# Kernel tuning notes

Hardware: AMD Instinct MI355X
Metric: run time of the kernel (lower is better)

## Reference

```python
import jax, jax.numpy as jnp
import numpy as np

B, T, N_EMBD, HEAD = 4, 4096, 1024, 64


def setup_inputs() -> dict:
    key = jax.random.key(0)
    kx, kk, kq, kv = jax.random.split(key, 4)
    x = jax.random.normal(kx, (B, T, N_EMBD), dtype=jnp.float32)
    s = 1.0 / np.sqrt(N_EMBD)  # init scale so activations stay O(1)
    Wk = jax.random.normal(kk, (N_EMBD, HEAD), dtype=jnp.float32) * s
    Wq = jax.random.normal(kq, (N_EMBD, HEAD), dtype=jnp.float32) * s
    Wv = jax.random.normal(kv, (N_EMBD, HEAD), dtype=jnp.float32) * s
    return {"x": x, "Wk": Wk, "Wq": Wq, "Wv": Wv}


def reference(x, Wk, Wq, Wv):
    Bd, Td, C = x.shape
    k = jnp.einsum('btc,ch->bth', x, Wk)
    q = jnp.einsum('btc,ch->bth', x, Wq)
    v = jnp.einsum('btc,ch->bth', x, Wv)
    # scores scaled by C**-0.5 where C = n_embd (as in the source, not head_size)
    w = jnp.einsum('bth,bsh->bts', q, k) * (C ** -0.5)
    causal = jnp.tril(jnp.ones((Td, Td), dtype=bool))  # [T, T]
    w = jnp.where(causal, w, -jnp.inf)
    w = jax.nn.softmax(w, axis=-1)
    out = jnp.einsum('bts,bsh->bth', w, v)  # [B, T, head_size]
    return out
```

## Files before the change

kernel.cpp:

```cpp
#include <hip/hip_runtime.h>
#include <cmath>

#define NB 4
#define NT 4096
#define NC 1024
#define NH 64
#define SCALE 0.03125f
#define MFIX 3.0f
#define LOG2E 1.4426950408889634f
#define NSPLIT 8
#define QE 1048576

typedef __attribute__((ext_vector_type(8))) short v8s;
typedef __attribute__((ext_vector_type(4))) float f32x4;

static __device__ __forceinline__ ushort f2bf(float x) {
    union { float f; uint u; } c; c.f = x;
    return (ushort)((c.u + 0x7FFF + ((c.u >> 16) & 1)) >> 16);
}
static __device__ __forceinline__ float bf2f(ushort h) {
    union { uint u; float f; } c; c.u = (uint)h << 16;
    return c.f;
}
static __device__ __forceinline__ uint pk2bf(float hi_f, float lo_f) {
    uint uh = __float_as_uint(hi_f) + 0x8000u;
    uint ul = __float_as_uint(lo_f) + 0x8000u;
    return __builtin_amdgcn_perm(uh, ul, 0x07060302u);
}

__global__ __launch_bounds__(256) void prep_kernel(
    const float* __restrict__ Wk, const float* __restrict__ Wq,
    const float* __restrict__ Wv, ushort* __restrict__ Wb)
{
    const int g    = blockIdx.x * 256 + threadIdx.x;
    const int lane = g & 63;
    const int kc   = (g >> 6) & 31;
    const int nt   = g >> 11;
    const int n    = nt * 16 + (lane & 15);
    const float* W = (n < 64) ? Wq : (n < 128) ? Wk : Wv;
    const int col  = n & 63;
    const int k0   = kc * 32 + ((lane >> 4) << 3);
    ushort t8[8];
    #pragma unroll
    for (int j = 0; j < 8; ++j)
        t8[j] = f2bf(W[(k0 + j) * 64 + col]);
    *(uint4*)(Wb + (size_t)g * 8) = *(const uint4*)t8;
}

#define PPAD 72

__global__ __launch_bounds__(256) void proj_kernel(
    const float* __restrict__ x, const ushort* __restrict__ Wb,
    ushort* __restrict__ qpack, ushort* __restrict__ kpack,
    ushort* __restrict__ vpack)
{
    __shared__ __align__(16) ushort As[2][32 * PPAD];
    __shared__ __align__(16) ushort Cs[32][200];

    const int tid  = threadIdx.x;
    const int w    = tid >> 6;
    const int lane = tid & 63;
    const int ln   = lane & 15;
    const int quad = lane >> 4;
    const long r0  = (long)blockIdx.x * 32;

    const int arow = tid >> 3, acol = (tid & 7) * 8;
    const float* xs = x + (r0 + arow) * NC + acol;

    const ushort* wb0 = Wb + (size_t)(w * 3 + 0) * 16384 + lane * 8;
    const ushort* wb1 = Wb + (size_t)(w * 3 + 1) * 16384 + lane * 8;
    const ushort* wb2 = Wb + (size_t)(w * 3 + 2) * 16384 + lane * 8;

    f32x4 acc[2][3];
    #pragma unroll
    for (int s = 0; s < 2; ++s)
        #pragma unroll
        for (int nt = 0; nt < 3; ++nt) acc[s][nt] = (f32x4){0.f,0.f,0.f,0.f};

    float4 f0 = *(const float4*)(xs);
    float4 f1 = *(const float4*)(xs + 4);
    float4 g0 = *(const float4*)(xs + 64);
    float4 g1 = *(const float4*)(xs + 68);
    v8s b[3][2];
    b[0][0] = *(const v8s*)(wb0);       b[0][1] = *(const v8s*)(wb0 + 512);
    b[1][0] = *(const v8s*)(wb1);       b[1][1] = *(const v8s*)(wb1 + 512);
    b[2][0] = *(const v8s*)(wb2);       b[2][1] = *(const v8s*)(wb2 + 512);
    {
        uint4 p = { pk2bf(f0.y, f0.x), pk2bf(f0.w, f0.z),
                    pk2bf(f1.y, f1.x), pk2bf(f1.w, f1.z) };
        *(uint4*)(&As[0][arow * PPAD + acol]) = p;
    }
    __syncthreads();

    int buf = 0;
    #pragma unroll
    for (int it = 0; it < 16; ++it) {
        float4 h0, h1;
        v8s nb[3][2];
        if (it < 14) {
            const int k2 = (it + 2) * 64;
            h0 = *(const float4*)(xs + k2);
            h1 = *(const float4*)(xs + k2 + 4);
        }
        if (it < 15) {
            const int off = (it + 1) * 1024;
            nb[0][0] = *(const v8s*)(wb0 + off); nb[0][1] = *(const v8s*)(wb0 + off + 512);
            nb[1][0] = *(const v8s*)(wb1 + off); nb[1][1] = *(const v8s*)(wb1 + off + 512);
            nb[2][0] = *(const v8s*)(wb2 + off); nb[2][1] = *(const v8s*)(wb2 + off + 512);
        }

        #pragma unroll
        for (int s = 0; s < 2; ++s) {
            const ushort* ap = &As[buf][(s * 16 + ln) * PPAD + quad * 8];
            v8s a0 = *(const v8s*)(ap);
            v8s a1 = *(const v8s*)(ap + 32);
            #pragma unroll
            for (int nt = 0; nt < 3; ++nt) {
                acc[s][nt] = __builtin_amdgcn_mfma_f32_16x16x32_bf16(a0, b[nt][0], acc[s][nt], 0, 0, 0);
                acc[s][nt] = __builtin_amdgcn_mfma_f32_16x16x32_bf16(a1, b[nt][1], acc[s][nt], 0, 0, 0);
            }
        }

        if (it < 15) {
            uint4 p = { pk2bf(g0.y, g0.x), pk2bf(g0.w, g0.z),
                        pk2bf(g1.y, g1.x), pk2bf(g1.w, g1.z) };
            *(uint4*)(&As[buf ^ 1][arow * PPAD + acol]) = p;
            #pragma unroll
            for (int nt = 0; nt < 3; ++nt) {
                b[nt][0] = nb[nt][0];
                b[nt][1] = nb[nt][1];
            }
        }
        if (it < 14) { g0 = h0; g1 = h1; }
        __syncthreads();
        buf ^= 1;
    }

    #pragma unroll
    for (int s = 0; s < 2; ++s)
        #pragma unroll
        for (int nt = 0; nt < 3; ++nt)
            #pragma unroll
            for (int r = 0; r < 4; ++r)
                Cs[s * 16 + quad * 4 + r][(w * 3 + nt) * 16 + ln] = f2bf(acc[s][nt][r]);
    __syncthreads();

    const int b_blk = (int)(r0 >> 12);
    const int t_loc = (int)(r0 & 4095);
    const int kt    = t_loc >> 6;
    const int kcb   = (t_loc >> 5) & 1;
    const int qt16a = t_loc >> 4;

    {
        const int f = tid >> 6, sx = f >> 1, kc = f & 1, lp = tid & 63;
        const int lnp = lp & 15, qdp = lp >> 4;
        const size_t fid = ((size_t)(b_blk * 256 + qt16a + sx) * 2 + kc);
        uint4 uq = *(const uint4*)(&Cs[sx * 16 + lnp][kc * 32 + qdp * 8]);
        *(uint4*)(qpack + fid * 512 + lp * 8) = uq;
        uint4 uk = *(const uint4*)(&Cs[sx * 16 + lnp][64 + kc * 32 + qdp * 8]);
        *(uint4*)(kpack + fid * 512 + lp * 8) = uk;
    }
    {
        const int td = tid >> 6, lp = tid & 63;
        const int lnv = lp & 15, qg = lp >> 4;
        ushort t8[8];
        #pragma unroll
        for (int j = 0; j < 8; ++j)
            t8[j] = Cs[qg * 8 + j][128 + td * 16 + lnv];
        const size_t fv = ((size_t)(b_blk * 64 + kt) * 2 + kcb) * 4 + td;
        *(uint4*)(vpack + fv * 512 + lp * 8) = *(const uint4*)t8;
    }
}

#define LPAD 72

__global__ __launch_bounds__(256) void attn_kernel(
    const ushort* __restrict__ qpack, const ushort* __restrict__ kpack,
    const ushort* __restrict__ vpack, ushort* __restrict__ Op,
    float* __restrict__ Lp)
{
    __shared__ __align__(16) ushort Ps[4][32 * LPAD];

    const int id = blockIdx.x;
    const int qt = 31 - (id / (4 * NSPLIT));
    const int c  = (id % (4 * NSPLIT)) >> 2;
    const int b  = id & 3;
    const int q0 = qt * 128;

    const int tid  = threadIdx.x;
    const int w    = tid >> 6;
    const int lane = tid & 63;
    const int ln   = lane & 15;
    const int quad = lane >> 4;
    const int qw0  = q0 + w * 32;
    const int qt16w = (qw0 >> 4);

    const ushort* qpb = qpack + (size_t)b * 256 * 2 * 512 + lane * 8;
    const ushort* kpb = kpack + (size_t)b * 64 * 8 * 512 + lane * 8;
    const ushort* vpb = vpack + (size_t)b * 64 * 8 * 512 + lane * 8;

    v8s qf[2][2];
    #pragma unroll
    for (int s = 0; s < 2; ++s) {
        qf[s][0] = *(const v8s*)(qpb + ((qt16w + s) * 2 + 0) * 512);
        qf[s][1] = *(const v8s*)(qpb + ((qt16w + s) * 2 + 1) * 512);
    }

    f32x4 o[2][4];
    #pragma unroll
    for (int s = 0; s < 2; ++s)
        #pragma unroll
        for (int td = 0; td < 4; ++td) o[s][td] = (f32x4){0.f,0.f,0.f,0.f};
    float l[2] = {0.f, 0.f};

    const int nkt   = 2 * qt + 2;
    const int cs    = (nkt + NSPLIT - 1) / NSPLIT;
    const int kt_lo = c * cs;
    const int kt_hi = min(nkt, kt_lo + cs);

    ushort* Pw = &Ps[w][0];

    for (int kt = kt_lo; kt < kt_hi; ++kt) {
        const ushort* kfb = kpb + (size_t)kt * 8 * 512;
        const ushort* vfb = vpb + (size_t)kt * 8 * 512;

        #pragma unroll
        for (int tk = 0; tk < 4; ++tk) {
            v8s kf0 = *(const v8s*)(kfb + (tk * 2 + 0) * 512);
            v8s kf1 = *(const v8s*)(kfb + (tk * 2 + 1) * 512);
            const int keybase = kt * 64 + tk * 16 + quad * 4;
            #pragma unroll
            for (int s = 0; s < 2; ++s) {
                f32x4 acc = (f32x4){0.f,0.f,0.f,0.f};
                acc = __builtin_amdgcn_mfma_f32_16x16x32_bf16(kf0, qf[s][0], acc, 0, 0, 0);
                acc = __builtin_amdgcn_mfma_f32_16x16x32_bf16(kf1, qf[s][1], acc, 0, 0, 0);
                const int qg = qw0 + s * 16 + ln;
                const bool needmask = (kt * 64 + 63) > (qw0 + s * 16);
                float p[4];
                #pragma unroll
                for (int r = 0; r < 4; ++r) {
                    float e = fmaf(acc[r], SCALE * LOG2E, -MFIX * LOG2E);
                    if (needmask && (keybase + r > qg)) e = -1e30f;
                    p[r] = __builtin_amdgcn_exp2f(e);
                    l[s] += p[r];
                }
                uint2 pw = { pk2bf(p[1], p[0]), pk2bf(p[3], p[2]) };
                *(uint2*)(&Pw[(s * 16 + ln) * LPAD + tk * 16 + quad * 4]) = pw;
            }
        }

        #pragma unroll
        for (int kc = 0; kc < 2; ++kc) {
            v8s vf[4];
            #pragma unroll
            for (int td = 0; td < 4; ++td)
                vf[td] = *(const v8s*)(vfb + (kc * 4 + td) * 512);
            #pragma unroll
            for (int s = 0; s < 2; ++s) {
                v8s pf = *(const v8s*)(&Pw[(s * 16 + ln) * LPAD + kc * 32 + quad * 8]);
                #pragma unroll
                for (int td = 0; td < 4; ++td)
                    o[s][td] = __builtin_amdgcn_mfma_f32_16x16x32_bf16(pf, vf[td], o[s][td], 0, 0, 0);
            }
        }
    }

    #pragma unroll
    for (int s = 0; s < 2; ++s) {
        l[s] += __shfl_xor(l[s], 16);
        l[s] += __shfl_xor(l[s], 32);
    }

    float* lpc = Lp + (size_t)c * NB * NT + (size_t)b * NT;
    const size_t obase = (((size_t)c * NB + b) * 32 + qt) * 4 + w;
    #pragma unroll
    for (int s = 0; s < 2; ++s) {
        if (quad == 0) lpc[qw0 + s * 16 + ln] = l[s];
        #pragma unroll
        for (int td = 0; td < 4; ++td) {
            uint2 pw = { pk2bf(o[s][td][1], o[s][td][0]),
                         pk2bf(o[s][td][3], o[s][td][2]) };
            *(uint2*)(Op + (((obase * 2 + s) * 4 + td) * 256 + lane * 4)) = pw;
        }
    }
}

__global__ __launch_bounds__(256) void combine_kernel(
    const ushort* __restrict__ Op, const float* __restrict__ Lp,
    float* __restrict__ out)
{
    const uint g   = blockIdx.x * 256 + threadIdx.x;
    const int lane = g & 63, ln = lane & 15, quad = lane >> 4;
    const int td   = (g >> 6) & 3;
    const int s    = (g >> 8) & 1;
    const int w    = (g >> 9) & 3;
    const int qt   = (g >> 11) & 31;
    const int b    = (g >> 16) & 3;
    const size_t QN = (size_t)NB * NT;

    const int q0 = qt * 128 + w * 32 + s * 16 + quad * 4;
    const size_t foff = ((((((size_t)b * 32 + qt) * 4 + w) * 2 + s) * 4 + td) * 256)
                        + lane * 4;

    float o0 = 0.f, o1 = 0.f, o2 = 0.f, o3 = 0.f;
    float L0 = 0.f, L1 = 0.f, L2 = 0.f, L3 = 0.f;
    #pragma unroll
    for (int c = 0; c < NSPLIT; ++c) {
        uint2 u = *(const uint2*)(Op + (size_t)c * QE + foff);
        o0 += bf2f((ushort)(u.x & 0xffff)); o1 += bf2f((ushort)(u.x >> 16));
        o2 += bf2f((ushort)(u.y & 0xffff)); o3 += bf2f((ushort)(u.y >> 16));
        float4 Lv = *(const float4*)(Lp + (size_t)c * QN + (size_t)b * NT + q0);
        L0 += Lv.x; L1 += Lv.y; L2 += Lv.z; L3 += Lv.w;
    }
    float* ob = out + ((size_t)b * NT + q0) * NH + td * 16 + ln;
    ob[0]   = o0 / L0;
    ob[64]  = o1 / L1;
    ob[128] = o2 / L2;
    ob[192] = o3 / L3;
}

extern "C" void kernel_launch(void* const* d_in, const int* in_sizes, int n_in,
                              void* d_out, int out_size, void* d_ws, size_t ws_size,
                              hipStream_t stream)
{
    const float* x  = (const float*)d_in[0];
    const float* Wk = (const float*)d_in[1];
    const float* Wq = (const float*)d_in[2];
    const float* Wv = (const float*)d_in[3];
    float* out = (float*)d_out;

    char* wsb = (char*)d_ws;
    ushort* qpack = (ushort*)wsb;
    ushort* kpack = qpack + QE;
    ushort* vpack = kpack + QE;
    ushort* Wb    = vpack + QE;
    ushort* Op    = (ushort*)(wsb + (8u << 20));
    float*  Lp    = (float*)(wsb + (40u << 20));

    prep_kernel<<<96, 256, 0, stream>>>(Wk, Wq, Wv, Wb);
    proj_kernel<<<NB * NT / 32, 256, 0, stream>>>(x, Wb, qpack, kpack, vpack);
    attn_kernel<<<32 * NSPLIT * NB, 256, 0, stream>>>(qpack, kpack, vpack, Op, Lp);
    combine_kernel<<<(int)(QE / 4 / 256), 256, 0, stream>>>(Op, Lp, out);
}
```

Before: 133.7 us.

## Fuse split-K combine into attention kernel via last-block atomic counter

Removes the separate combine kernel launch. Each attention block atomically increments a per-(batch, query-tile) counter after writing its partials, and the last of the NSPLIT blocks reduces the partial outputs and row sums and writes the final normalized output. Counters are zeroed in the prep kernel. This saves a launch and lets the combine overlap with other attention blocks, at the cost of fences, an atomic per block, and serialized tail work in the last-arriving block.

Result: slower. 301.8 us (+125.7%).

```diff
diff --git a/kernel.cpp b/kernel.cpp
--- a/kernel.cpp
+++ b/kernel.cpp
@@ -30,9 +30,11 @@
 
 __global__ __launch_bounds__(256) void prep_kernel(
     const float* __restrict__ Wk, const float* __restrict__ Wq,
-    const float* __restrict__ Wv, ushort* __restrict__ Wb)
+    const float* __restrict__ Wv, ushort* __restrict__ Wb,
+    int* __restrict__ cnt)
 {
     const int g    = blockIdx.x * 256 + threadIdx.x;
+    if (g < NB * 32) cnt[g] = 0;
     const int lane = g & 63;
     const int kc   = (g >> 6) & 31;
     const int nt   = g >> 11;
@@ -177,9 +179,12 @@
 __global__ __launch_bounds__(256) void attn_kernel(
     const ushort* __restrict__ qpack, const ushort* __restrict__ kpack,
     const ushort* __restrict__ vpack, ushort* __restrict__ Op,
-    float* __restrict__ Lp)
+    float* __restrict__ Lp, int* __restrict__ cnt,
+    float* __restrict__ out)
 {
     __shared__ __align__(16) ushort Ps[4][32 * LPAD];
+    __shared__ float Lsum[128];
+    __shared__ int lastFlag;
 
     const int id = blockIdx.x;
     const int qt = 31 - (id / (4 * NSPLIT));
@@ -283,40 +288,51 @@
             *(uint2*)(Op + (((obase * 2 + s) * 4 + td) * 256 + lane * 4)) = pw;
         }
     }
-}
-
-__global__ __launch_bounds__(256) void combine_kernel(
-    const ushort* __restrict__ Op, const float* __restrict__ Lp,
-    float* __restrict__ out)
-{
-    const uint g   = blockIdx.x * 256 + threadIdx.x;
-    const int lane = g & 63, ln = lane & 15, quad = lane >> 4;
-    const int td   = (g >> 6) & 3;
-    const int s    = (g >> 8) & 1;
-    const int w    = (g >> 9) & 3;
-    const int qt   = (g >> 11) & 31;
-    const int b    = (g >> 16) & 3;
+
+    __threadfence();
+    __syncthreads();
+    if (tid == 0) {
+        int old = __hip_atomic_fetch_add(&cnt[b * 32 + qt], 1,
+                                         __ATOMIC_ACQ_REL, __HIP_MEMORY_SCOPE_AGENT);
+        lastFlag = (old == NSPLIT - 1);
+    }
+    __syncthreads();
+    if (!lastFlag) return;
+    __threadfence();
+
     const size_t QN = (size_t)NB * NT;
-
-    const int q0 = qt * 128 + w * 32 + s * 16 + quad * 4;
-    const size_t foff = ((((((size_t)b * 32 + qt) * 4 + w) * 2 + s) * 4 + td) * 256)
-                        + lane * 4;
-
-    float o0 = 0.f, o1 = 0.f, o2 = 0.f, o3 = 0.f;
-    float L0 = 0.f, L1 = 0.f, L2 = 0.f, L3 = 0.f;
-    #pragma unroll
-    for (int c = 0; c < NSPLIT; ++c) {
-        uint2 u = *(const uint2*)(Op + (size_t)c * QE + foff);
-        o0 += bf2f((ushort)(u.x & 0xffff)); o1 += bf2f((ushort)(u.x >> 16));
-        o2 += bf2f((ushort)(u.y & 0xffff)); o3 += bf2f((ushort)(u.y >> 16));
-        float4 Lv = *(const float4*)(Lp + (size_t)c * QN + (size_t)b * NT + q0);
-        L0 += Lv.x; L1 += Lv.y; L2 += Lv.z; L3 += Lv.w;
-    }
-    float* ob = out + ((size_t)b * NT + q0) * NH + td * 16 + ln;
-    ob[0]   = o0 / L0;
-    ob[64]  = o1 / L1;
-    ob[128] = o2 / L2;
-    ob[192] = o3 / L3;
+    if (tid < 128) {
+        float Ls = 0.f;
+        #pragma unroll
+        for (int cc = 0; cc < NSPLIT; ++cc)
+            Ls += Lp[(size_t)cc * QN + (size_t)b * NT + q0 + tid];
+        Lsum[tid] = Ls;
+    }
+    __syncthreads();
+
+    #pragma unroll
+    for (int u = 0; u < 8; ++u) {
+        const int loc = u * 256 + tid;
+        const int w2  = loc >> 9;
+        const int s2  = (loc >> 8) & 1;
+        const int td2 = (loc >> 6) & 3;
+        const int ln2 = loc & 63;
+        const size_t foff = ((((((size_t)b * 32 + qt) * 4 + w2) * 2 + s2) * 4 + td2) * 256)
+                            + ln2 * 4;
+        float o0 = 0.f, o1 = 0.f, o2 = 0.f, o3 = 0.f;
+        #pragma unroll
+        for (int cc = 0; cc < NSPLIT; ++cc) {
+            uint2 u2 = *(const uint2*)(Op + (size_t)cc * QE + foff);
+            o0 += bf2f((ushort)(u2.x & 0xffff)); o1 += bf2f((ushort)(u2.x >> 16));
+            o2 += bf2f((ushort)(u2.y & 0xffff)); o3 += bf2f((ushort)(u2.y >> 16));
+        }
+        const int qr = w2 * 32 + s2 * 16 + (ln2 >> 4) * 4;
+        float* ob = out + ((size_t)b * NT + q0 + qr) * NH + td2 * 16 + (ln2 & 15);
+        ob[0]      = o0 / Lsum[qr];
+        ob[NH]     = o1 / Lsum[qr + 1];
+        ob[2 * NH] = o2 / Lsum[qr + 2];
+        ob[3 * NH] = o3 / Lsum[qr + 3];
+    }
 }
 
 extern "C" void kernel_launch(void* const* d_in, const int* in_sizes, int n_in,
@@ -336,9 +352,9 @@
     ushort* Wb    = vpack + QE;
     ushort* Op    = (ushort*)(wsb + (8u << 20));
     float*  Lp    = (float*)(wsb + (40u << 20));
-
-    prep_kernel<<<96, 256, 0, stream>>>(Wk, Wq, Wv, Wb);
+    int*    cnt   = (int*)(wsb + (44u << 20));
+
+    prep_kernel<<<96, 256, 0, stream>>>(Wk, Wq, Wv, Wb, cnt);
     proj_kernel<<<NB * NT / 32, 256, 0, stream>>>(x, Wb, qpack, kpack, vpack);
-    attn_kernel<<<32 * NSPLIT * NB, 256, 0, stream>>>(qpack, kpack, vpack, Op, Lp);
-    combine_kernel<<<(int)(QE / 4 / 256), 256, 0, stream>>>(Op, Lp, out);
-}
+    attn_kernel<<<32 * NSPLIT * NB, 256, 0, stream>>>(qpack, kpack, vpack, Op, Lp, cnt, out);
+}
```

## Replace global split-K attention and combine kernel with in-block key split

Applied to the files above, without the earlier changes.

The attention kernel no longer splits keys across eight blocks with bf16 partials and a separate combine kernel. Each block now owns a pair of 32-row query tiles (j and 127-j) to balance causal work. Its four waves stride over 32-key tiles and reduce their partial O and L through shared memory, then write the normalized fp32 output directly. This drops the partial-result global traffic and one launch, but grid size falls to 256 blocks, each with a serial two-phase loop and fewer waves per query.

Result: slower. 137.5 us (+2.8%).

```diff
diff --git a/kernel.cpp b/kernel.cpp
--- a/kernel.cpp
+++ b/kernel.cpp
@@ -8,7 +8,6 @@
 #define SCALE 0.03125f
 #define MFIX 3.0f
 #define LOG2E 1.4426950408889634f
-#define NSPLIT 8
 #define QE 1048576
 
 typedef __attribute__((ext_vector_type(8))) short v8s;
@@ -17,10 +16,6 @@
 static __device__ __forceinline__ ushort f2bf(float x) {
     union { float f; uint u; } c; c.f = x;
     return (ushort)((c.u + 0x7FFF + ((c.u >> 16) & 1)) >> 16);
-}
-static __device__ __forceinline__ float bf2f(ushort h) {
-    union { uint u; float f; } c; c.u = (uint)h << 16;
-    return c.f;
 }
 static __device__ __forceinline__ uint pk2bf(float hi_f, float lo_f) {
     uint uh = __float_as_uint(hi_f) + 0x8000u;
@@ -172,151 +167,132 @@
     }
 }
 
-#define LPAD 72
+#define LPAD 40
 
 __global__ __launch_bounds__(256) void attn_kernel(
     const ushort* __restrict__ qpack, const ushort* __restrict__ kpack,
-    const ushort* __restrict__ vpack, ushort* __restrict__ Op,
-    float* __restrict__ Lp)
+    const ushort* __restrict__ vpack, float* __restrict__ out)
 {
     __shared__ __align__(16) ushort Ps[4][32 * LPAD];
+    __shared__ __align__(16) float Obuf[4][32][68];
+    __shared__ float Lbuf[4][32];
 
     const int id = blockIdx.x;
-    const int qt = 31 - (id / (4 * NSPLIT));
-    const int c  = (id % (4 * NSPLIT)) >> 2;
+    const int j  = id >> 2;
     const int b  = id & 3;
-    const int q0 = qt * 128;
 
     const int tid  = threadIdx.x;
     const int w    = tid >> 6;
     const int lane = tid & 63;
     const int ln   = lane & 15;
     const int quad = lane >> 4;
-    const int qw0  = q0 + w * 32;
-    const int qt16w = (qw0 >> 4);
 
     const ushort* qpb = qpack + (size_t)b * 256 * 2 * 512 + lane * 8;
-    const ushort* kpb = kpack + (size_t)b * 64 * 8 * 512 + lane * 8;
-    const ushort* vpb = vpack + (size_t)b * 64 * 8 * 512 + lane * 8;
-
-    v8s qf[2][2];
-    #pragma unroll
-    for (int s = 0; s < 2; ++s) {
-        qf[s][0] = *(const v8s*)(qpb + ((qt16w + s) * 2 + 0) * 512);
-        qf[s][1] = *(const v8s*)(qpb + ((qt16w + s) * 2 + 1) * 512);
-    }
-
-    f32x4 o[2][4];
-    #pragma unroll
-    for (int s = 0; s < 2; ++s)
-        #pragma unroll
-        for (int td = 0; td < 4; ++td) o[s][td] = (f32x4){0.f,0.f,0.f,0.f};
-    float l[2] = {0.f, 0.f};
-
-    const int nkt   = 2 * qt + 2;
-    const int cs    = (nkt + NSPLIT - 1) / NSPLIT;
-    const int kt_lo = c * cs;
-    const int kt_hi = min(nkt, kt_lo + cs);
+    const ushort* kpb = kpack + (size_t)b * 256 * 2 * 512 + lane * 8;
+    const ushort* vpb = vpack + (size_t)b * 128 * 4 * 512 + lane * 8;
 
     ushort* Pw = &Ps[w][0];
 
-    for (int kt = kt_lo; kt < kt_hi; ++kt) {
-        const ushort* kfb = kpb + (size_t)kt * 8 * 512;
-        const ushort* vfb = vpb + (size_t)kt * 8 * 512;
-
-        #pragma unroll
-        for (int tk = 0; tk < 4; ++tk) {
-            v8s kf0 = *(const v8s*)(kfb + (tk * 2 + 0) * 512);
-            v8s kf1 = *(const v8s*)(kfb + (tk * 2 + 1) * 512);
-            const int keybase = kt * 64 + tk * 16 + quad * 4;
+    #pragma unroll
+    for (int ph = 0; ph < 2; ++ph) {
+        const int jp = ph ? (127 - j) : j;
+        const int q0 = jp * 32;
+
+        v8s qf[2][2];
+        #pragma unroll
+        for (int s = 0; s < 2; ++s) {
+            qf[s][0] = *(const v8s*)(qpb + ((size_t)((jp * 2 + s) * 2 + 0)) * 512);
+            qf[s][1] = *(const v8s*)(qpb + ((size_t)((jp * 2 + s) * 2 + 1)) * 512);
+        }
+
+        f32x4 o[2][4];
+        #pragma unroll
+        for (int s = 0; s < 2; ++s)
+            #pragma unroll
+            for (int td = 0; td < 4; ++td) o[s][td] = (f32x4){0.f,0.f,0.f,0.f};
+        float l[2] = {0.f, 0.f};
+
+        for (int kk = w; kk <= jp; kk += 4) {
+            const ushort* kfb = kpb + (size_t)kk * 4 * 512;
+            const ushort* vfb = vpb + (size_t)kk * 4 * 512;
+            const bool diag = (kk == jp);
+
+            #pragma unroll
+            for (int tk = 0; tk < 2; ++tk) {
+                v8s kf0 = *(const v8s*)(kfb + (tk * 2 + 0) * 512);
+                v8s kf1 = *(const v8s*)(kfb + (tk * 2 + 1) * 512);
+                const int keybase = kk * 32 + tk * 16 + quad * 4;
+                #pragma unroll
+                for (int s = 0; s < 2; ++s) {
+                    f32x4 acc = (f32x4){0.f,0.f,0.f,0.f};
+                    acc = __builtin_amdgcn_mfma_f32_16x16x32_bf16(kf0, qf[s][0], acc, 0, 0, 0);
+                    acc = __builtin_amdgcn_mfma_f32_16x16x32_bf16(kf1, qf[s][1], acc, 0, 0, 0);
+                    const int qg = q0 + s * 16 + ln;
+                    float p[4];
+                    #pragma unroll
+                    for (int r = 0; r < 4; ++r) {
+                        float e = fmaf(acc[r], SCALE * LOG2E, -MFIX * LOG2E);
+                        if (diag && (keybase + r > qg)) e = -1e30f;
+                        p[r] = __builtin_amdgcn_exp2f(e);
+                        l[s] += p[r];
+                    }
+                    uint2 pw = { pk2bf(p[1], p[0]), pk2bf(p[3], p[2]) };
+                    *(uint2*)(&Pw[(s * 16 + ln) * LPAD + tk * 16 + quad * 4]) = pw;
+                }
+            }
+
+            v8s vf[4];
+            #pragma unroll
+            for (int td = 0; td < 4; ++td)
+                vf[td] = *(const v8s*)(vfb + td * 512);
             #pragma unroll
             for (int s = 0; s < 2; ++s) {
-                f32x4 acc = (f32x4){0.f,0.f,0.f,0.f};
-                acc = __builtin_amdgcn_mfma_f32_16x16x32_bf16(kf0, qf[s][0], acc, 0, 0, 0);
-                acc = __builtin_amdgcn_mfma_f32_16x16x32_bf16(kf1, qf[s][1], acc, 0, 0, 0);
-                const int qg = qw0 + s * 16 + ln;
-                const bool needmask = (kt * 64 + 63) > (qw0 + s * 16);
-                float p[4];
-                #pragma unroll
-                for (int r = 0; r < 4; ++r) {
-                    float e = fmaf(acc[r], SCALE * LOG2E, -MFIX * LOG2E);
-                    if (needmask && (keybase + r > qg)) e = -1e30f;
-                    p[r] = __builtin_amdgcn_exp2f(e);
-                    l[s] += p[r];
-                }
-                uint2 pw = { pk2bf(p[1], p[0]), pk2bf(p[3], p[2]) };
-                *(uint2*)(&Pw[(s * 16 + ln) * LPAD + tk * 16 + quad * 4]) = pw;
-            }
-        }
-
-        #pragma unroll
-        for (int kc = 0; kc < 2; ++kc) {
-            v8s vf[4];
-            #pragma unroll
-            for (int td = 0; td < 4; ++td)
-                vf[td] = *(const v8s*)(vfb + (kc * 4 + td) * 512);
-            #pragma unroll
-            for (int s = 0; s < 2; ++s) {
-                v8s pf = *(const v8s*)(&Pw[(s * 16 + ln) * LPAD + kc * 32 + quad * 8]);
+                v8s pf = *(const v8s*)(&Pw[(s * 16 + ln) * LPAD + quad * 8]);
                 #pragma unroll
                 for (int td = 0; td < 4; ++td)
                     o[s][td] = __builtin_amdgcn_mfma_f32_16x16x32_bf16(pf, vf[td], o[s][td], 0, 0, 0);
             }
         }
-    }
-
-    #pragma unroll
-    for (int s = 0; s < 2; ++s) {
-        l[s] += __shfl_xor(l[s], 16);
-        l[s] += __shfl_xor(l[s], 32);
-    }
-
-    float* lpc = Lp + (size_t)c * NB * NT + (size_t)b * NT;
-    const size_t obase = (((size_t)c * NB + b) * 32 + qt) * 4 + w;
-    #pragma unroll
-    for (int s = 0; s < 2; ++s) {
-        if (quad == 0) lpc[qw0 + s * 16 + ln] = l[s];
-        #pragma unroll
-        for (int td = 0; td < 4; ++td) {
-            uint2 pw = { pk2bf(o[s][td][1], o[s][td][0]),
-                         pk2bf(o[s][td][3], o[s][td][2]) };
-            *(uint2*)(Op + (((obase * 2 + s) * 4 + td) * 256 + lane * 4)) = pw;
-        }
-    }
-}
-
-__global__ __launch_bounds__(256) void combine_kernel(
-    const ushort* __restrict__ Op, const float* __restrict__ Lp,
-    float* __restrict__ out)
-{
-    const uint g   = blockIdx.x * 256 + threadIdx.x;
-    const int lane = g & 63, ln = lane & 15, quad = lane >> 4;
-    const int td   = (g >> 6) & 3;
-    const int s    = (g >> 8) & 1;
-    const int w    = (g >> 9) & 3;
-    const int qt   = (g >> 11) & 31;
-    const int b    = (g >> 16) & 3;
-    const size_t QN = (size_t)NB * NT;
-
-    const int q0 = qt * 128 + w * 32 + s * 16 + quad * 4;
-    const size_t foff = ((((((size_t)b * 32 + qt) * 4 + w) * 2 + s) * 4 + td) * 256)
-                        + lane * 4;
-
-    float o0 = 0.f, o1 = 0.f, o2 = 0.f, o3 = 0.f;
-    float L0 = 0.f, L1 = 0.f, L2 = 0.f, L3 = 0.f;
-    #pragma unroll
-    for (int c = 0; c < NSPLIT; ++c) {
-        uint2 u = *(const uint2*)(Op + (size_t)c * QE + foff);
-        o0 += bf2f((ushort)(u.x & 0xffff)); o1 += bf2f((ushort)(u.x >> 16));
-        o2 += bf2f((ushort)(u.y & 0xffff)); o3 += bf2f((ushort)(u.y >> 16));
-        float4 Lv = *(const float4*)(Lp + (size_t)c * QN + (size_t)b * NT + q0);
-        L0 += Lv.x; L1 += Lv.y; L2 += Lv.z; L3 += Lv.w;
-    }
-    float* ob = out + ((size_t)b * NT + q0) * NH + td * 16 + ln;
-    ob[0]   = o0 / L0;
-    ob[64]  = o1 / L1;
-    ob[128] = o2 / L2;
-    ob[192] = o3 / L3;
+
+        #pragma unroll
+        for (int s = 0; s < 2; ++s) {
+            l[s] += __shfl_xor(l[s], 16);
+            l[s] += __shfl_xor(l[s], 32);
+        }
+
+        #pragma unroll
+        for (int s = 0; s < 2; ++s) {
+            #pragma unroll
+            for (int td = 0; td < 4; ++td)
+                #pragma unroll
+                for (int r = 0; r < 4; ++r)
+                    Obuf[w][s * 16 + quad * 4 + r][td * 16 + ln] = o[s][td][r];
+            if (quad == 0) Lbuf[w][s * 16 + ln] = l[s];
+        }
+        __syncthreads();
+
+        {
+            const int qr = tid >> 3;
+            const int h0 = (tid & 7) * 8;
+            float s0=0.f,s1=0.f,s2=0.f,s3=0.f,s4=0.f,s5=0.f,s6=0.f,s7=0.f,Ls=0.f;
+            #pragma unroll
+            for (int ww = 0; ww < 4; ++ww) {
+                const float* Or = &Obuf[ww][qr][h0];
+                float4 u = *(const float4*)(Or);
+                float4 v2 = *(const float4*)(Or + 4);
+                s0 += u.x;  s1 += u.y;  s2 += u.z;  s3 += u.w;
+                s4 += v2.x; s5 += v2.y; s6 += v2.z; s7 += v2.w;
+                Ls += Lbuf[ww][qr];
+            }
+            const float inv = 1.0f / Ls;
+            float4 r0 = { s0 * inv, s1 * inv, s2 * inv, s3 * inv };
+            float4 r1 = { s4 * inv, s5 * inv, s6 * inv, s7 * inv };
+            float* ob = out + ((size_t)b * NT + q0 + qr) * NH + h0;
+            *(float4*)(ob)     = r0;
+            *(float4*)(ob + 4) = r1;
+        }
+        __syncthreads();
+    }
 }
 
 extern "C" void kernel_launch(void* const* d_in, const int* in_sizes, int n_in,
@@ -334,11 +310,8 @@
     ushort* kpack = qpack + QE;
     ushort* vpack = kpack + QE;
     ushort* Wb    = vpack + QE;
-    ushort* Op    = (ushort*)(wsb + (8u << 20));
-    float*  Lp    = (float*)(wsb + (40u << 20));
 
     prep_kernel<<<96, 256, 0, stream>>>(Wk, Wq, Wv, Wb);
     proj_kernel<<<NB * NT / 32, 256, 0, stream>>>(x, Wb, qpack, kpack, vpack);
-    attn_kernel<<<32 * NSPLIT * NB, 256, 0, stream>>>(qpack, kpack, vpack, Op, Lp);
-    combine_kernel<<<(int)(QE / 4 / 256), 256, 0, stream>>>(Op, Lp, out);
-}
+    attn_kernel<<<64 * NB, 256, 0, stream>>>(qpack, kpack, vpack, out);
+}
```
